# Kernel optimization log

Measured on AMD Instinct MI355X. Metric: run time of the kernel, lower is better.

The kernel has to match this reference:

```python
import jax, jax.numpy as jnp
import numpy as np

T, B, I, H, O_FREQ, O_CTX = 1024, 32, 64, 1024, 64, 8
ALPHA = 0.1  # leak rate
G = 1.5      # chaotic gain used by init_weights


def setup_inputs() -> dict:
    key = jax.random.key(0)
    ks = jax.random.split(key, 8)
    std1 = G / np.sqrt(H)  # init_weights scaling

    def centered_normal(k, shape, std):
        w = jax.random.normal(k, shape, dtype=jnp.float32)
        return (w - w.mean()) * std

    input_sig = jax.random.normal(ks[0], (T, B, I), dtype=jnp.float32)
    rate = jax.random.uniform(ks[1], (B, H), dtype=jnp.float32, minval=-1.0, maxval=1.0)
    i2h_w = centered_normal(ks[2], (H, I), std1)
    i2h_b = jnp.zeros((H,), dtype=jnp.float32)
    h2h_w = centered_normal(ks[3], (H, H), std1)
    h2h_b = jnp.zeros((H,), dtype=jnp.float32)
    h2o_w = centered_normal(ks[4], (O_FREQ, H), std1)
    h2o_b = jnp.zeros((O_FREQ,), dtype=jnp.float32)
    h2o_ctx_w = jax.random.normal(ks[5], (O_CTX, H), dtype=jnp.float32)
    h2o_ctx_b = jnp.zeros((O_CTX,), dtype=jnp.float32)
    return {
        "input_sig": input_sig, "rate": rate,
        "i2h_w": i2h_w, "i2h_b": i2h_b,
        "h2h_w": h2h_w, "h2h_b": h2h_b,
        "h2o_w": h2o_w, "h2o_b": h2o_b,
        "h2o_ctx_w": h2o_ctx_w, "h2o_ctx_b": h2o_ctx_b,
    }


def reference(input_sig, rate, i2h_w, i2h_b, h2h_w, h2h_b,
              h2o_w, h2o_b, h2o_ctx_w, h2o_ctx_b):
    # forward_dual: leaky-tanh recurrence over T steps, then both readouts.
    # Precompute all input projections in one big GEMM: [T,B,H]
    x_proj = jnp.einsum('tbi,hi->tbh', input_sig, i2h_w) + i2h_b

    def step(r, xp):
        pre = xp + r @ h2h_w.T + h2h_b  # i2h(x_t) + h2h(r)  (no noise)
        r_new = (1.0 - ALPHA) * r + ALPHA * jnp.tanh(pre)
        return r_new, r_new

    _, rate_all = jax.lax.scan(step, rate, x_proj)  # [T,B,H]
    output = jnp.einsum('tbh,oh->tbo', rate_all, h2o_w) + h2o_b
    output_ctx = jnp.einsum('tbh,ch->tbc', rate_all, h2o_ctx_w) + h2o_ctx_b
    return (output, output_ctx, rate_all)
```

## Files before the change

kernel.cpp:

```cpp
#include <hip/hip_runtime.h>

constexpr int T  = 1024;
constexpr int B  = 32;
constexpr int I_ = 64;
constexpr int H  = 1024;
constexpr int OF = 64;
constexpr int OC = 8;
constexpr int NG = 16;
constexpr int NM = 16;
constexpr int CH  = 136;
constexpr int CHP = 140;
constexpr int BSTR = 8 * CHP;
constexpr long long OUT1_OFF = (long long)T * B * OF;
constexpr long long OUT2_OFF = (long long)T * B * (OF + OC);
constexpr int RING_U64 = NG * 2 * 2 * 1024;

__device__ __forceinline__ void st_agent_u64(unsigned long long* p,
                                             unsigned long long v) {
  __hip_atomic_store(p, v, __ATOMIC_RELAXED, __HIP_MEMORY_SCOPE_AGENT);
}
__device__ __forceinline__ unsigned long long
ld_agent_u64(const unsigned long long* p) {
  return __hip_atomic_load(p, __ATOMIC_RELAXED, __HIP_MEMORY_SCOPE_AGENT);
}

__global__ __launch_bounds__(512, 2) void rnn_recur(
    const float* __restrict__ input_sig, const float* __restrict__ rate0,
    const float* __restrict__ i2h_w, const float* __restrict__ i2h_b,
    const float* __restrict__ h2h_w, const float* __restrict__ h2h_b,
    float* __restrict__ rate_all, unsigned long long* __restrict__ ring)
{
  const int tid = threadIdx.x;
  const int bid = blockIdx.x;
  const int g   = bid & (NG - 1);
  const int m   = bid >> 4;
  const int l8  = tid & 7;
  const int jrel = tid >> 3;
  const int j   = m * 64 + jrel;
  const int bG  = g * 2;

  __shared__ float lds[2][BSTR];

  float4 w4[34];
#pragma unroll
  for (int q = 0; q < 34; ++q) {
    const int k = l8 * CH + q * 4;
    w4[q] = (k < H) ? *(const float4*)(h2h_w + (long long)j * H + k)
                    : *(const float4*)(i2h_w + (long long)j * I_ + (k - H));
  }
  const float bsum = h2h_b[j] + i2h_b[j];
  const int posj = (j / CH) * CHP + (j % CH);

  {
    const int b = tid >> 8, u4 = tid & 255;
    const int k0 = u4 * 4, c = k0 / CH, off = k0 - c * CH;
    float4 v = *(const float4*)(rate0 + (long long)(bG + b) * H + k0);
    *(float4*)&lds[b][c * CHP + off] = v;
    if (tid < 32) {
      const int b2 = tid >> 4, iq = tid & 15;
      float4 u = *(const float4*)(input_sig + (long long)(bG + b2) * I_ + iq * 4);
      *(float4*)&lds[b2][7 * CHP + 72 + iq * 4] = u;
    }
  }
  __syncthreads();

  unsigned long long* ringG = ring + (long long)g * (2 * 2 * 1024);

  auto phase = [&](int b, int t) {
    const float* Rb = &lds[b][0];
    float acc = 0.f;
#pragma unroll
    for (int q = 0; q < 34; ++q) {
      const float4 rv = *(const float4*)&Rb[l8 * CHP + q * 4];
      acc = fmaf(w4[q].x, rv.x, acc);
      acc = fmaf(w4[q].y, rv.y, acc);
      acc = fmaf(w4[q].z, rv.z, acc);
      acc = fmaf(w4[q].w, rv.w, acc);
    }
    acc += __shfl_xor(acc, 4, 64);
    acc += __shfl_xor(acc, 2, 64);
    acc += __shfl_xor(acc, 1, 64);
    if (l8 == 0) {
      const float pre  = acc + bsum;
      const float rold = Rb[posj];
      const float rnew = 0.9f * rold + 0.1f * tanhf(pre);
      const unsigned long long pkt =
          ((unsigned long long)(unsigned)(t + 1) << 32) |
          (unsigned long long)__float_as_uint(rnew);
      st_agent_u64(&ringG[((long long)((t & 1) * 2 + b) << 10) + j], pkt);
      rate_all[((long long)t * B + bG + b) * H + j] = rnew;
    }
  };

  auto probe = [&](int b, unsigned tag, int slot, int xt) {
    float4 xv;
    const bool xs = (tid < 16);
    if (xs) {
      xv = *(const float4*)(input_sig + ((long long)xt * B + bG + b) * I_ + tid * 4);
    }
    const unsigned long long* p = &ringG[((long long)(slot * 2 + b) << 10) + 2 * tid];
    unsigned long long v0 = ld_agent_u64(p);
    unsigned long long v1 = ld_agent_u64(p + 1);
    while ((unsigned)(v0 >> 32) != tag || (unsigned)(v1 >> 32) != tag) {
      v0 = ld_agent_u64(p);
      v1 = ld_agent_u64(p + 1);
    }
    const int c = (2 * tid) / CH, off = 2 * tid - c * CH;
    *(float2*)&lds[b][c * CHP + off] = make_float2(
        __uint_as_float((unsigned)v0), __uint_as_float((unsigned)v1));
    if (xs) *(float4*)&lds[b][7 * CHP + 72 + tid * 4] = xv;
  };

  for (int t = 0; t < T; ++t) {
    phase(0, t);
    if (t > 0) probe(1, (unsigned)t, (t - 1) & 1, t);
    __syncthreads();
    phase(1, t);
    if (t + 1 < T) probe(0, (unsigned)(t + 1), t & 1, t + 1);
    __syncthreads();
  }
}

__global__ __launch_bounds__(256) void rnn_readout(
    const float* __restrict__ rate_all,
    const float* __restrict__ h2o_w, const float* __restrict__ h2o_b,
    const float* __restrict__ h2o_ctx_w, const float* __restrict__ h2o_ctx_b,
    float* __restrict__ out0, float* __restrict__ out1)
{
  constexpr int RB = 128;
  constexpr int HC = 128;
  constexpr int SR = HC + 1;
  __shared__ float rl[RB * SR];
  __shared__ float wl[72 * SR];

  const int tid = threadIdx.x;
  const long long row0 = (long long)blockIdx.x * RB;
  const int rb = tid & 31, og = tid >> 5;

  float acc[4][9];
#pragma unroll
  for (int c = 0; c < 4; ++c)
#pragma unroll
    for (int i = 0; i < 9; ++i) acc[c][i] = 0.f;

  for (int hc = 0; hc < H / HC; ++hc) {
#pragma unroll
    for (int i = 0; i < 16; ++i) {
      const int q = i * 256 + tid;
      const int row = q >> 5, hq = q & 31;
      float4 v = *(const float4*)(rate_all + (row0 + row) * H + hc * HC + hq * 4);
      float* d = &rl[row * SR + hq * 4];
      d[0] = v.x; d[1] = v.y; d[2] = v.z; d[3] = v.w;
    }
#pragma unroll
    for (int i = 0; i < 9; ++i) {
      const int q = i * 256 + tid;
      const int o = q >> 5, hq = q & 31;
      const float* src = (o < OF) ? (h2o_w + (long long)o * H)
                                  : (h2o_ctx_w + (long long)(o - OF) * H);
      float4 v = *(const float4*)(src + hc * HC + hq * 4);
      float* d = &wl[o * SR + hq * 4];
      d[0] = v.x; d[1] = v.y; d[2] = v.z; d[3] = v.w;
    }
    __syncthreads();

#pragma unroll 4
    for (int h = 0; h < HC; ++h) {
      const float r0 = rl[(rb)      * SR + h];
      const float r1 = rl[(rb + 32) * SR + h];
      const float r2 = rl[(rb + 64) * SR + h];
      const float r3 = rl[(rb + 96) * SR + h];
#pragma unroll
      for (int i = 0; i < 9; ++i) {
        const float wv = wl[(og * 9 + i) * SR + h];
        acc[0][i] = fmaf(r0, wv, acc[0][i]);
        acc[1][i] = fmaf(r1, wv, acc[1][i]);
        acc[2][i] = fmaf(r2, wv, acc[2][i]);
        acc[3][i] = fmaf(r3, wv, acc[3][i]);
      }
    }
    __syncthreads();
  }

#pragma unroll
  for (int c = 0; c < 4; ++c) {
    const long long row = row0 + rb + 32 * c;
#pragma unroll
    for (int i = 0; i < 9; ++i) {
      const int o = og * 9 + i;
      if (o < OF) out0[row * OF + o] = acc[c][i] + h2o_b[o];
      else        out1[row * OC + (o - OF)] = acc[c][i] + h2o_ctx_b[o - OF];
    }
  }
}

extern "C" void kernel_launch(void* const* d_in, const int* in_sizes, int n_in,
                              void* d_out, int out_size, void* d_ws, size_t ws_size,
                              hipStream_t stream) {
  (void)in_sizes; (void)n_in; (void)d_ws; (void)ws_size; (void)out_size;
  const float* input_sig = (const float*)d_in[0];
  const float* rate0     = (const float*)d_in[1];
  const float* i2h_w     = (const float*)d_in[2];
  const float* i2h_b     = (const float*)d_in[3];
  const float* h2h_w     = (const float*)d_in[4];
  const float* h2h_b     = (const float*)d_in[5];
  const float* h2o_w     = (const float*)d_in[6];
  const float* h2o_b     = (const float*)d_in[7];
  const float* h2o_ctx_w = (const float*)d_in[8];
  const float* h2o_ctx_b = (const float*)d_in[9];

  float* out      = (float*)d_out;
  float* out0     = out;
  float* out1     = out + OUT1_OFF;
  float* rate_all = out + OUT2_OFF;
  unsigned long long* ring = (unsigned long long*)d_out;

  hipMemsetAsync(ring, 0, (size_t)RING_U64 * 8, stream);
  hipLaunchKernelGGL(rnn_recur, dim3(NG * NM), dim3(512), 0, stream,
                     input_sig, rate0, i2h_w, i2h_b, h2h_w, h2h_b,
                     rate_all, ring);
  hipLaunchKernelGGL(rnn_readout, dim3(256), dim3(256), 0, stream,
                     rate_all, h2o_w, h2o_b, h2o_ctx_w, h2o_ctx_b, out0, out1);
}
```

Before: 2.872 ms.

## Issue ring polls before matvec and use packed FMA in recurrence

The first poll of the neighbour-exchange ring and the input-signal load for the other batch are now issued before the current phase's matvec, so their latency overlaps with compute, and the spin loop only runs afterwards. The weight registers are regrouped as float2 pairs and the dot product uses two-wide elementwise FMA, which is meant to map onto packed FP32 FMA instructions. The early poll may read stale tags more often and then fall back to spinning. Splitting the accumulator into two lanes slightly changes the floating-point summation order.

```diff
diff --git a/kernel.cpp b/kernel.cpp
--- a/kernel.cpp
+++ b/kernel.cpp
@@ -1,4 +1,7 @@
 #include <hip/hip_runtime.h>
+
+typedef float v2f __attribute__((ext_vector_type(2)));
+typedef float v4f __attribute__((ext_vector_type(4)));
 
 constexpr int T  = 1024;
 constexpr int B  = 32;
@@ -41,12 +44,12 @@
 
   __shared__ float lds[2][BSTR];
 
-  float4 w4[34];
-#pragma unroll
-  for (int q = 0; q < 34; ++q) {
-    const int k = l8 * CH + q * 4;
-    w4[q] = (k < H) ? *(const float4*)(h2h_w + (long long)j * H + k)
-                    : *(const float4*)(i2h_w + (long long)j * I_ + (k - H));
+  v2f w2[68];
+#pragma unroll
+  for (int q = 0; q < 68; ++q) {
+    const int k = l8 * CH + q * 2;
+    w2[q] = (k < H) ? *(const v2f*)(h2h_w + (long long)j * H + k)
+                    : *(const v2f*)(i2h_w + (long long)j * I_ + (k - H));
   }
   const float bsum = h2h_b[j] + i2h_b[j];
   const int posj = (j / CH) * CHP + (j % CH);
@@ -65,18 +68,21 @@
   __syncthreads();
 
   unsigned long long* ringG = ring + (long long)g * (2 * 2 * 1024);
+  const int c_  = (2 * tid) / CH;
+  const int off_ = 2 * tid - c_ * CH;
 
   auto phase = [&](int b, int t) {
     const float* Rb = &lds[b][0];
-    float acc = 0.f;
+    v2f acc2 = {0.f, 0.f};
 #pragma unroll
     for (int q = 0; q < 34; ++q) {
-      const float4 rv = *(const float4*)&Rb[l8 * CHP + q * 4];
-      acc = fmaf(w4[q].x, rv.x, acc);
-      acc = fmaf(w4[q].y, rv.y, acc);
-      acc = fmaf(w4[q].z, rv.z, acc);
-      acc = fmaf(w4[q].w, rv.w, acc);
-    }
+      const v4f rv = *(const v4f*)&Rb[l8 * CHP + q * 4];
+      const v2f rlo = __builtin_shufflevector(rv, rv, 0, 1);
+      const v2f rhi = __builtin_shufflevector(rv, rv, 2, 3);
+      acc2 = __builtin_elementwise_fma(w2[2 * q],     rlo, acc2);
+      acc2 = __builtin_elementwise_fma(w2[2 * q + 1], rhi, acc2);
+    }
+    float acc = acc2.x + acc2.y;
     acc += __shfl_xor(acc, 4, 64);
     acc += __shfl_xor(acc, 2, 64);
     acc += __shfl_xor(acc, 1, 64);
@@ -92,31 +98,61 @@
     }
   };
 
-  auto probe = [&](int b, unsigned tag, int slot, int xt) {
-    float4 xv;
-    const bool xs = (tid < 16);
-    if (xs) {
-      xv = *(const float4*)(input_sig + ((long long)xt * B + bG + b) * I_ + tid * 4);
-    }
-    const unsigned long long* p = &ringG[((long long)(slot * 2 + b) << 10) + 2 * tid];
-    unsigned long long v0 = ld_agent_u64(p);
-    unsigned long long v1 = ld_agent_u64(p + 1);
-    while ((unsigned)(v0 >> 32) != tag || (unsigned)(v1 >> 32) != tag) {
-      v0 = ld_agent_u64(p);
-      v1 = ld_agent_u64(p + 1);
-    }
-    const int c = (2 * tid) / CH, off = 2 * tid - c * CH;
-    *(float2*)&lds[b][c * CHP + off] = make_float2(
-        __uint_as_float((unsigned)v0), __uint_as_float((unsigned)v1));
-    if (xs) *(float4*)&lds[b][7 * CHP + 72 + tid * 4] = xv;
-  };
-
   for (int t = 0; t < T; ++t) {
+    unsigned long long v10 = 0, v11 = 0;
+    float4 xv1;
+    const bool have1 = (t > 0);
+    const unsigned long long* p1 =
+        &ringG[((long long)((((t - 1) & 1) * 2) + 1) << 10) + 2 * tid];
+    if (have1) {
+      v10 = ld_agent_u64(p1);
+      v11 = ld_agent_u64(p1 + 1);
+      if (tid < 16) {
+        xv1 = *(const float4*)(input_sig +
+            ((long long)t * B + bG + 1) * I_ + tid * 4);
+      }
+    }
+
     phase(0, t);
-    if (t > 0) probe(1, (unsigned)t, (t - 1) & 1, t);
-    __syncthreads();
+
+    if (have1) {
+      const unsigned tag = (unsigned)t;
+      while ((unsigned)(v10 >> 32) != tag || (unsigned)(v11 >> 32) != tag) {
+        v10 = ld_agent_u64(p1);
+        v11 = ld_agent_u64(p1 + 1);
+      }
+      *(float2*)&lds[1][c_ * CHP + off_] = make_float2(
+          __uint_as_float((unsigned)v10), __uint_as_float((unsigned)v11));
+      if (tid < 16) *(float4*)&lds[1][7 * CHP + 72 + tid * 4] = xv1;
+    }
+    __syncthreads();
+
+    unsigned long long v00 = 0, v01 = 0;
+    float4 xv0;
+    const bool have0 = (t + 1 < T);
+    const unsigned long long* p0 =
+        &ringG[((long long)((t & 1) * 2) << 10) + 2 * tid];
+    if (have0) {
+      v00 = ld_agent_u64(p0);
+      v01 = ld_agent_u64(p0 + 1);
+      if (tid < 16) {
+        xv0 = *(const float4*)(input_sig +
+            ((long long)(t + 1) * B + bG) * I_ + tid * 4);
+      }
+    }
+
     phase(1, t);
-    if (t + 1 < T) probe(0, (unsigned)(t + 1), t & 1, t + 1);
+
+    if (have0) {
+      const unsigned tag = (unsigned)(t + 1);
+      while ((unsigned)(v00 >> 32) != tag || (unsigned)(v01 >> 32) != tag) {
+        v00 = ld_agent_u64(p0);
+        v01 = ld_agent_u64(p0 + 1);
+      }
+      *(float2*)&lds[0][c_ * CHP + off_] = make_float2(
+          __uint_as_float((unsigned)v00), __uint_as_float((unsigned)v01));
+      if (tid < 16) *(float4*)&lds[0][7 * CHP + 72 + tid * 4] = xv0;
+    }
     __syncthreads();
   }
 }
```

After: 2.507 ms. 1.15x faster.

## Regroup recurrent kernel into 8 batch groups of 4 with 1024-thread blocks

Applied to the files above, without the earlier changes.

Restructures the persistent recurrence so each block handles 4 batch rows (8 groups × 32 column blocks) with 1024 threads, where 32 lanes split each hidden row's dot product using packed float2 FMAs and a 5-step shuffle reduction. The ring exchange becomes a 4-slot pipeline: the remote load for a batch row is issued before computing the current row and awaited afterwards, overlapping inter-block communication with compute. This is meant to cut per-step synchronisation and spin latency and to use packed FMA throughput. In exchange it holds fewer weights per thread, does more shuffle work, runs one block per CU, and adds a __syncthreads per batch row.

```diff
diff --git a/kernel.cpp b/kernel.cpp
--- a/kernel.cpp
+++ b/kernel.cpp
@@ -1,4 +1,6 @@
 #include <hip/hip_runtime.h>
+
+typedef float v2f __attribute__((ext_vector_type(2)));
 
 constexpr int T  = 1024;
 constexpr int B  = 32;
@@ -6,14 +8,11 @@
 constexpr int H  = 1024;
 constexpr int OF = 64;
 constexpr int OC = 8;
-constexpr int NG = 16;
-constexpr int NM = 16;
-constexpr int CH  = 136;
-constexpr int CHP = 140;
-constexpr int BSTR = 8 * CHP;
+constexpr int NGR = 8;
+constexpr int NMEM = 32;
 constexpr long long OUT1_OFF = (long long)T * B * OF;
 constexpr long long OUT2_OFF = (long long)T * B * (OF + OC);
-constexpr int RING_U64 = NG * 2 * 2 * 1024;
+constexpr int RING_U64 = 2 * NGR * 4 * 1024;
 
 __device__ __forceinline__ void st_agent_u64(unsigned long long* p,
                                              unsigned long long v) {
@@ -24,7 +23,7 @@
   return __hip_atomic_load(p, __ATOMIC_RELAXED, __HIP_MEMORY_SCOPE_AGENT);
 }
 
-__global__ __launch_bounds__(512, 2) void rnn_recur(
+__global__ __launch_bounds__(1024, 1) void rnn_recur(
     const float* __restrict__ input_sig, const float* __restrict__ rate0,
     const float* __restrict__ i2h_w, const float* __restrict__ i2h_b,
     const float* __restrict__ h2h_w, const float* __restrict__ h2h_b,
@@ -32,92 +31,87 @@
 {
   const int tid = threadIdx.x;
   const int bid = blockIdx.x;
-  const int g   = bid & (NG - 1);
-  const int m   = bid >> 4;
-  const int l8  = tid & 7;
-  const int jrel = tid >> 3;
-  const int j   = m * 64 + jrel;
-  const int bG  = g * 2;
-
-  __shared__ float lds[2][BSTR];
-
-  float4 w4[34];
-#pragma unroll
-  for (int q = 0; q < 34; ++q) {
-    const int k = l8 * CH + q * 4;
-    w4[q] = (k < H) ? *(const float4*)(h2h_w + (long long)j * H + k)
-                    : *(const float4*)(i2h_w + (long long)j * I_ + (k - H));
+  const int g   = bid & (NGR - 1);
+  const int m   = bid >> 3;
+  const int r   = tid >> 5;
+  const int s   = tid & 31;
+  const int j   = m * 32 + r;
+  const int bG  = g * 4;
+
+  __shared__ float lds[4][1088];
+
+  v2f w2[17];
+#pragma unroll
+  for (int q = 0; q < 17; ++q) {
+    const int k = q * 64 + 2 * s;
+    w2[q] = (q < 16) ? *(const v2f*)(h2h_w + (long long)j * H + k)
+                     : *(const v2f*)(i2h_w + (long long)j * I_ + (k - H));
   }
   const float bsum = h2h_b[j] + i2h_b[j];
-  const int posj = (j / CH) * CHP + (j % CH);
-
-  {
-    const int b = tid >> 8, u4 = tid & 255;
-    const int k0 = u4 * 4, c = k0 / CH, off = k0 - c * CH;
-    float4 v = *(const float4*)(rate0 + (long long)(bG + b) * H + k0);
-    *(float4*)&lds[b][c * CHP + off] = v;
-    if (tid < 32) {
-      const int b2 = tid >> 4, iq = tid & 15;
-      float4 u = *(const float4*)(input_sig + (long long)(bG + b2) * I_ + iq * 4);
-      *(float4*)&lds[b2][7 * CHP + 72 + iq * 4] = u;
-    }
+
+#pragma unroll
+  for (int y = 0; y < 4; ++y) {
+    lds[y][tid] = rate0[(long long)(bG + y) * H + tid];
+  }
+  if (tid < 256) {
+    const int y = tid >> 6, xi = tid & 63;
+    lds[y][1024 + xi] = input_sig[(long long)(bG + y) * I_ + xi];
   }
   __syncthreads();
 
-  unsigned long long* ringG = ring + (long long)g * (2 * 2 * 1024);
-
-  auto phase = [&](int b, int t) {
-    const float* Rb = &lds[b][0];
-    float acc = 0.f;
-#pragma unroll
-    for (int q = 0; q < 34; ++q) {
-      const float4 rv = *(const float4*)&Rb[l8 * CHP + q * 4];
-      acc = fmaf(w4[q].x, rv.x, acc);
-      acc = fmaf(w4[q].y, rv.y, acc);
-      acc = fmaf(w4[q].z, rv.z, acc);
-      acc = fmaf(w4[q].w, rv.w, acc);
-    }
-    acc += __shfl_xor(acc, 4, 64);
-    acc += __shfl_xor(acc, 2, 64);
-    acc += __shfl_xor(acc, 1, 64);
-    if (l8 == 0) {
-      const float pre  = acc + bsum;
-      const float rold = Rb[posj];
-      const float rnew = 0.9f * rold + 0.1f * tanhf(pre);
-      const unsigned long long pkt =
-          ((unsigned long long)(unsigned)(t + 1) << 32) |
-          (unsigned long long)__float_as_uint(rnew);
-      st_agent_u64(&ringG[((long long)((t & 1) * 2 + b) << 10) + j], pkt);
-      rate_all[((long long)t * B + bG + b) * H + j] = rnew;
-    }
-  };
-
-  auto probe = [&](int b, unsigned tag, int slot, int xt) {
-    float4 xv;
-    const bool xs = (tid < 16);
-    if (xs) {
-      xv = *(const float4*)(input_sig + ((long long)xt * B + bG + b) * I_ + tid * 4);
-    }
-    const unsigned long long* p = &ringG[((long long)(slot * 2 + b) << 10) + 2 * tid];
-    unsigned long long v0 = ld_agent_u64(p);
-    unsigned long long v1 = ld_agent_u64(p + 1);
-    while ((unsigned)(v0 >> 32) != tag || (unsigned)(v1 >> 32) != tag) {
-      v0 = ld_agent_u64(p);
-      v1 = ld_agent_u64(p + 1);
-    }
-    const int c = (2 * tid) / CH, off = 2 * tid - c * CH;
-    *(float2*)&lds[b][c * CHP + off] = make_float2(
-        __uint_as_float((unsigned)v0), __uint_as_float((unsigned)v1));
-    if (xs) *(float4*)&lds[b][7 * CHP + 72 + tid * 4] = xv;
-  };
+  unsigned long long* ringBase = ring;
 
   for (int t = 0; t < T; ++t) {
-    phase(0, t);
-    if (t > 0) probe(1, (unsigned)t, (t - 1) & 1, t);
-    __syncthreads();
-    phase(1, t);
-    if (t + 1 < T) probe(0, (unsigned)(t + 1), t & 1, t + 1);
-    __syncthreads();
+#pragma unroll
+    for (int y = 0; y < 4; ++y) {
+      const int p  = (y + 2) & 3;
+      const int tp = (y < 2) ? t - 1 : t;
+      const bool doR = (tp >= 0) && (tp <= T - 2);
+      unsigned long long pkt = 0;
+      float4 xv;
+      const bool xs = (tid < 16);
+      const unsigned long long* ap =
+          ringBase + ((((long long)(tp & 1) * NGR + g) * 4 + p) << 10) + tid;
+      if (doR) {
+        pkt = ld_agent_u64(ap);
+        if (xs) {
+          xv = *(const float4*)(input_sig +
+              ((long long)(tp + 1) * B + bG + p) * I_ + tid * 4);
+        }
+      }
+
+      v2f acc2 = {0.f, 0.f};
+#pragma unroll
+      for (int q = 0; q < 17; ++q) {
+        const v2f rv = *(const v2f*)&lds[y][q * 64 + 2 * s];
+        acc2 = __builtin_elementwise_fma(w2[q], rv, acc2);
+      }
+      float acc = acc2.x + acc2.y;
+      acc += __shfl_xor(acc, 16, 64);
+      acc += __shfl_xor(acc, 8, 64);
+      acc += __shfl_xor(acc, 4, 64);
+      acc += __shfl_xor(acc, 2, 64);
+      acc += __shfl_xor(acc, 1, 64);
+      if (s == 0) {
+        const float pre  = acc + bsum;
+        const float rold = lds[y][j];
+        const float rnew = 0.9f * rold + 0.1f * tanhf(pre);
+        const unsigned long long out =
+            ((unsigned long long)(unsigned)(t + 1) << 32) |
+            (unsigned long long)__float_as_uint(rnew);
+        st_agent_u64(ringBase +
+            ((((long long)(t & 1) * NGR + g) * 4 + y) << 10) + j, out);
+        rate_all[((long long)t * B + bG + y) * H + j] = rnew;
+      }
+
+      if (doR) {
+        const unsigned tag = (unsigned)(tp + 1);
+        while ((unsigned)(pkt >> 32) != tag) pkt = ld_agent_u64(ap);
+        lds[p][tid] = __uint_as_float((unsigned)pkt);
+        if (xs) *(float4*)&lds[p][1024 + tid * 4] = xv;
+      }
+      __syncthreads();
+    }
   }
 }
 
@@ -216,7 +210,7 @@
   unsigned long long* ring = (unsigned long long*)d_out;
 
   hipMemsetAsync(ring, 0, (size_t)RING_U64 * 8, stream);
-  hipLaunchKernelGGL(rnn_recur, dim3(NG * NM), dim3(512), 0, stream,
+  hipLaunchKernelGGL(rnn_recur, dim3(NGR * NMEM), dim3(1024), 0, stream,
                      input_sig, rate0, i2h_w, i2h_b, h2h_w, h2h_b,
                      rate_all, ring);
   hipLaunchKernelGGL(rnn_readout, dim3(256), dim3(256), 0, stream,
```

After: 6.137 ms. +113.7%, slower.
